# Performance work log

Hardware: AMD Instinct MI355X
Metric: run time of the kernel (lower is better)

Reference implementation:

```python
import jax, jax.numpy as jnp
import numpy as np

EMB = 128
EA = 32
ET = 32
NN = 50000
NE = 320000
NBAND = 3
LAM = 0.01  # softshrink sparsity_threshold
LN_EPS = 1e-5


def _softshrink(x, lam=LAM):
    return jnp.where(x > lam, x - lam, jnp.where(x < -lam, x + lam, jnp.zeros_like(x)))


def _forward(hidden, edge_attr, edge_time_emb, boundary_condition,
             alpha, r1, i1, rb1, ib1, fre_w, fre_b,
             comb_w, comb_b, lin_w, lin_b, ln_g, ln_b, edge_index):
    num_nodes = hidden.shape[0]
    # gather source node features and concat edge features -> [E, d_in]
    x = jnp.concatenate([hidden[edge_index[0]], edge_attr, edge_time_emb], axis=1)
    # FreMLP: FFT over feature dim (real input -> complex64)
    x_fft = jnp.fft.fft(x)
    xr, xi = x_fft.real, x_fft.imag
    energy = jnp.sum(xr * xr + xi * xi, axis=-1)  # [E]
    energy_sum = jnp.sum(energy)
    outs = []
    for k in range(NBAND):
        factor = (2.0 * (k + 1) - 1.0) / (2.0 * NBAND)
        Qk = alpha[k] * factor * energy_sum
        bk = energy_sum / (alpha[k] * (2.0 * NBAND))
        mask = ((energy >= Qk - bk) & (energy <= Qk + bk)).astype(x.dtype)[:, None]
        fr = xr * mask
        fi = xi * mask
        # complex linear: (fr + i*fi) @ (r1 + i*i1) + (rb1 + i*ib1)
        o_r = fr @ r1[k] - fi @ i1[k] + rb1[k]
        o_i = fi @ r1[k] + fr @ i1[k] + ib1[k]
        o_r = _softshrink(jax.nn.relu(o_r))
        o_i = _softshrink(jax.nn.relu(o_i))
        outs.append(jax.lax.complex(o_r, o_i))
    y_fft = jnp.concatenate(outs, axis=-1)  # [E, NBAND*EMB] complex
    y = jnp.fft.ifft(y_fft).real
    msg = y @ fre_w + fre_b  # [E, EMB]
    # view_as_complex(msg, 0) -> view_as_real -> flatten: interleave real with zeros
    msg_ri = jnp.stack([msg, jnp.zeros_like(msg)], axis=-1).reshape(msg.shape[0], 2 * EMB)
    msg2 = msg_ri @ comb_w + comb_b  # [E, EMB]
    # scatter-reduce(sum) into destination nodes + boundary self-loops
    msg_aug = jnp.concatenate([msg2, boundary_condition], axis=0)
    idx_aug = jnp.concatenate([edge_index[1], jnp.arange(num_nodes, dtype=edge_index.dtype)])
    out = jax.ops.segment_sum(msg_aug, idx_aug, num_segments=num_nodes)
    out = out @ lin_w + lin_b
    mu = jnp.mean(out, axis=-1, keepdims=True)
    var = jnp.mean((out - mu) ** 2, axis=-1, keepdims=True)
    out = (out - mu) * jax.lax.rsqrt(var + LN_EPS) * ln_g + ln_b
    return jax.nn.relu(out)  # dropout is identity in eval mode


def setup_inputs() -> dict:
    key = jax.random.key(0)
    ks = jax.random.split(key, 16)
    d_in = EMB + EA + ET
    s = 0.02
    return {
        "hidden": jax.random.normal(ks[0], (NN, EMB), jnp.float32),
        "edge_attr": jax.random.normal(ks[1], (NE, EA), jnp.float32),
        "edge_time_emb": jax.random.normal(ks[2], (NE, ET), jnp.float32),
        "boundary_condition": jax.random.normal(ks[3], (NN, EMB), jnp.float32),
        "alpha": jnp.ones((NBAND,), jnp.float32),
        "r1": s * jax.random.normal(ks[4], (NBAND, d_in, EMB), jnp.float32),
        "i1": s * jax.random.normal(ks[5], (NBAND, d_in, EMB), jnp.float32),
        "rb1": s * jax.random.normal(ks[6], (NBAND, EMB), jnp.float32),
        "ib1": s * jax.random.normal(ks[7], (NBAND, EMB), jnp.float32),
        "fre_w": s * jax.random.normal(ks[8], (NBAND * EMB, EMB), jnp.float32),
        "fre_b": s * jax.random.normal(ks[9], (EMB,), jnp.float32),
        "comb_w": s * jax.random.normal(ks[10], (2 * EMB, EMB), jnp.float32),
        "comb_b": s * jax.random.normal(ks[11], (EMB,), jnp.float32),
        "lin_w": s * jax.random.normal(ks[12], (EMB, EMB), jnp.float32),
        "lin_b": s * jax.random.normal(ks[13], (EMB,), jnp.float32),
        "ln_g": jnp.ones((EMB,), jnp.float32),
        "ln_b": jnp.zeros((EMB,), jnp.float32),
        "edge_index": jax.random.randint(ks[14], (2, NE), 0, NN, dtype=jnp.int32),
    }


def reference(hidden, edge_attr, edge_time_emb, boundary_condition, alpha, r1, i1, rb1, ib1,
              fre_w, fre_b, comb_w, comb_b, lin_w, lin_b, ln_g, ln_b, edge_index):
    return _forward(hidden, edge_attr, edge_time_emb, boundary_condition, alpha, r1, i1,
                    rb1, ib1, fre_w, fre_b, comb_w, comb_b, lin_w, lin_b, ln_g, ln_b, edge_index)
```

## Files before the change

kernel.cpp:

```cpp
#include <hip/hip_runtime.h>
#include <hip/hip_bf16.h>

#define NNODES 50000
#define NEDGES 320000
#define EMB 128
#define DIN 192
#define NB 3
#define LAM 0.01f
#define LN_EPS 1e-5f
#define PI_F 3.14159265358979323846f

#define SCAN_B 196
#define SCAN_N (SCAN_B * 256)

typedef __attribute__((ext_vector_type(8))) short v8s;
typedef __attribute__((ext_vector_type(4))) float v4f;
typedef __attribute__((ext_vector_type(2))) float v2f;

#define WS_ESUM 0
#define WS_WB   16
#define WS_G2B  (WS_WB + 73728)
#define WS_G2   (WS_G2B + 49152)
#define WS_PHI  (WS_G2 + 98304)
#define WS_M    (WS_PHI + 98304)
#define WS_BB   (WS_M + 16384)
#define WS_GB2  (WS_BB + 768)
#define WS_CK   (WS_GB2 + 128)
#define WS_EN   (WS_CK + 384)
#define WS_NORM (WS_EN + NEDGES)
#define WS_CNT  (WS_NORM + NNODES)
#define WS_CUR  (WS_CNT + SCAN_N)
#define WS_PART (WS_CUR + SCAN_N)
#define WS_EIDS (WS_PART + 256)

__device__ __forceinline__ unsigned pk2(float a, float b) {
  __hip_bfloat162 h2 = __float22bfloat162_rn(make_float2(a, b));
  return *reinterpret_cast<unsigned*>(&h2);
}

__device__ __forceinline__ void atomic2(float* dp, float a, float b) {
#if __has_builtin(__builtin_amdgcn_flat_atomic_fadd_v2f32)
  v2f val; val.x = a; val.y = b;
  __builtin_amdgcn_flat_atomic_fadd_v2f32((v2f*)dp, val);
#else
  atomicAdd(dp, a); atomicAdd(dp + 1, b);
#endif
}

__global__ __launch_bounds__(256) void k_prep1(
    const float* __restrict__ r1, const float* __restrict__ i1,
    __hip_bfloat16* __restrict__ Wb, const float* __restrict__ comb_w,
    const float* __restrict__ lin_w, float* __restrict__ M,
    const float* __restrict__ fre_w, float* __restrict__ Phi,
    const float* __restrict__ hidden, float* __restrict__ norms) {
  __shared__ float cs[384], sn[384];
  const int t = threadIdx.x;
  const int b = blockIdx.x;
  if (b < 576) {
    if (t < 192) sincosf((2.f * PI_F / 192.f) * (float)t, &sn[t], &cs[t]);
    __syncthreads();
    int idx = b * 256 + t;
    int n = idx / 768, c = idx - (idx / 768) * 768;
    int k = c >> 8, col = c & 255;
    int isI = col >> 7, j = col & 127;
    const float* ap = (isI ? i1 : r1) + (size_t)k * DIN * EMB + j;
    const float* bp = (isI ? r1 : i1) + (size_t)k * DIN * EMB + j;
    float sgn = isI ? -1.f : 1.f;
    float acc = 0.f;
    int m = 0;
    for (int f = 0; f < DIN; ++f) {
      acc = fmaf(cs[m], ap[(size_t)f * EMB], fmaf(sgn * sn[m], bp[(size_t)f * EMB], acc));
      m += n; if (m >= 192) m -= 192;
    }
    int kc = n >> 5, quad = (n & 31) >> 3, jj = n & 7;
    int lane = quad * 16 + (col & 15);
    Wb[((((k * 6 + kc) * 16 + (col >> 4)) * 64) + lane) * 8 + jj] = __float2bfloat16(acc);
  } else if (b < 640) {
    int idx = (b - 576) * 256 + t;
    int j = idx >> 7, j2 = idx & 127;
    float acc = 0.f;
    for (int tt = 0; tt < 128; ++tt)
      acc = fmaf(comb_w[(2 * j) * 128 + tt], lin_w[tt * 128 + j2], acc);
    M[idx] = acc;
  } else if (b < 1024) {
    for (int i = t; i < 384; i += 256)
      sincosf((2.f * PI_F / 384.f) * (float)i, &sn[i], &cs[i]);
    __syncthreads();
    int idx = (b - 640) * 256 + t;
    int slot = idx >> 7, j1 = idx & 127;
    int k = slot >> 8, r = slot & 255;
    int isI = r >> 7;
    int f = k * 128 + (r & 127);
    const float* tp = isI ? sn : cs;
    float sg = isI ? -1.f : 1.f;
    float acc = 0.f;
    int m = 0;
    for (int n = 0; n < 384; ++n) {
      acc = fmaf(sg * tp[m], fre_w[n * 128 + j1], acc);
      m += f; if (m >= 384) m -= 384;
    }
    Phi[slot * 128 + j1] = acc * (1.f / 384.f);
  } else {
    const int w = t >> 6, lane = t & 63;
    const int n = (b - 1024) * 4 + w;
    const float2 v = ((const float2*)(hidden + (size_t)n * 128))[lane];
    float ss = v.x * v.x + v.y * v.y;
#pragma unroll
    for (int off = 32; off > 0; off >>= 1) ss += __shfl_xor(ss, off, 64);
    if (lane == 0) norms[n] = ss;
  }
}

__global__ __launch_bounds__(256) void k_prep2(
    const float* __restrict__ Phi, const float* __restrict__ M,
    float* __restrict__ G2, __hip_bfloat16* __restrict__ G2b,
    const float* __restrict__ norms, const float* __restrict__ eattr,
    const float* __restrict__ ett, const int* __restrict__ eidx,
    float* __restrict__ energies, float* __restrict__ esum,
    int* __restrict__ cnt) {
  const int t = threadIdx.x;
  const int b = blockIdx.x;
  if (b < 384) {
    int idx = b * 256 + t;
    int slot = idx >> 7, j2 = idx & 127;
    float acc = 0.f;
    for (int j1 = 0; j1 < 128; ++j1)
      acc = fmaf(Phi[slot * 128 + j1], M[j1 * 128 + j2], acc);
    G2[idx] = acc;
    int k = slot >> 8, s = slot & 255;
    int kc = s >> 5, quad = (s & 31) >> 3, jj = s & 7;
    G2b[((((k * 8 + kc) * 8 + (j2 >> 4)) * 64) + quad * 16 + (j2 & 15)) * 8 + jj] =
        __float2bfloat16(acc);
  } else {
    int e = (b - 384) * 256 + t;
    float ss = norms[eidx[e]];
    const float4* a4 = (const float4*)(eattr + (size_t)e * 32);
#pragma unroll
    for (int i = 0; i < 8; ++i) {
      float4 v = a4[i];
      ss += v.x * v.x + v.y * v.y + v.z * v.z + v.w * v.w;
    }
    const float4* t4 = (const float4*)(ett + (size_t)e * 32);
#pragma unroll
    for (int i = 0; i < 8; ++i) {
      float4 v = t4[i];
      ss += v.x * v.x + v.y * v.y + v.z * v.z + v.w * v.w;
    }
    float en = 192.f * ss;
    energies[e] = en;
    float tot = en;
#pragma unroll
    for (int off = 32; off > 0; off >>= 1) tot += __shfl_down(tot, off, 64);
    if ((t & 63) == 0) atomicAdd(esum, tot);
    atomicAdd(&cnt[eidx[NEDGES + e]], 1);
  }
}

__global__ __launch_bounds__(256) void k_prep3(
    const float* __restrict__ rb1, const float* __restrict__ ib1,
    const float* __restrict__ fre_b, const float* __restrict__ comb_b,
    const float* __restrict__ lin_w, const float* __restrict__ M,
    const float* __restrict__ G2, float* __restrict__ bb,
    float* __restrict__ gb2, float* __restrict__ ck,
    int* __restrict__ cnt, int* __restrict__ part) {
  __shared__ int sm[256];
  const int t = threadIdx.x;
  const int b = blockIdx.x;
  if (b < 5) {
    int idx = b * 256 + t;
    if (idx < 768) {
      int k = idx >> 8, r = idx & 255;
      bb[idx] = (r >= 128) ? ib1[k * 128 + (r & 127)] : rb1[k * 128 + r];
    } else if (idx < 896) {
      int j2 = idx - 768;
      float acc = 0.f;
      for (int j = 0; j < 128; ++j) acc += fre_b[j] * M[j * 128 + j2];
      for (int tt = 0; tt < 128; ++tt) acc += comb_b[tt] * lin_w[tt * 128 + j2];
      gb2[j2] = acc;
    } else if (idx < 1280) {
      int q = idx - 896;
      int k = q >> 7, j2 = q & 127;
      float acc = 0.f;
      for (int j = 0; j < 128; ++j) {
        float vr = rb1[k * 128 + j];
        vr = fmaxf(vr, 0.f); vr = (vr > LAM) ? vr - LAM : 0.f;
        float vi = ib1[k * 128 + j];
        vi = fmaxf(vi, 0.f); vi = (vi > LAM) ? vi - LAM : 0.f;
        acc += vr * G2[(k * 256 + j) * 128 + j2] + vi * G2[(k * 256 + 128 + j) * 128 + j2];
      }
      ck[k * 128 + j2] = acc;
    }
  } else {
    int blk = b - 5;
    int i = blk * 256 + t;
    int v = (i < NNODES) ? cnt[i] : 0;
    sm[t] = v;
    __syncthreads();
#pragma unroll
    for (int off = 1; off < 256; off <<= 1) {
      int x = (t >= off) ? sm[t - off] : 0;
      __syncthreads();
      sm[t] += x;
      __syncthreads();
    }
    cnt[i] = sm[t] - v;
    if (t == 255) part[blk] = sm[t];
  }
}

__global__ __launch_bounds__(256) void k_scanB(int* __restrict__ part) {
  __shared__ int sm[256];
  const int t = threadIdx.x;
  int v = (t < SCAN_B) ? part[t] : 0;
  sm[t] = v;
  __syncthreads();
#pragma unroll
  for (int off = 1; off < 256; off <<= 1) {
    int x = (t >= off) ? sm[t - off] : 0;
    __syncthreads();
    sm[t] += x;
    __syncthreads();
  }
  if (t < SCAN_B) part[t] = sm[t] - v;
}

__global__ __launch_bounds__(256) void k_scanC(const int* __restrict__ scanned,
                                               const int* __restrict__ part,
                                               int* __restrict__ cur) {
  int i = blockIdx.x * 256 + threadIdx.x;
  cur[i] = scanned[i] + part[blockIdx.x];
}

__global__ __launch_bounds__(256) void k_fill(const int* __restrict__ eidx,
                                              int* __restrict__ cur,
                                              int* __restrict__ eids) {
  int e = blockIdx.x * 256 + threadIdx.x;
  int pos = atomicAdd(&cur[eidx[NEDGES + e]], 1);
  eids[pos] = e;
}

#define XS_STR 200
#define OS_STR 264
#define ZS_STR 130
__global__ __launch_bounds__(512, 4) void k_edges(
    const float* __restrict__ hidden, const float* __restrict__ eattr,
    const float* __restrict__ ett, const float* __restrict__ alpha,
    const int* __restrict__ eidx, const int* __restrict__ eids,
    const __hip_bfloat16* __restrict__ Wb, const __hip_bfloat16* __restrict__ G2b,
    const float* __restrict__ bb, const float* __restrict__ gb2,
    const float* __restrict__ ck, const float* __restrict__ energies,
    const float* __restrict__ esum, float* __restrict__ accum) {
  __shared__ __align__(16) char smem[64 * XS_STR * 2 + 64 * OS_STR * 2];
  short* Xs = (short*)smem;
  short* Os = (short*)(smem + 64 * XS_STR * 2);
  float* Zs = (float*)smem;
  __shared__ float maskf[3][64];
  __shared__ int eid_s[64], srcs[64], dsts[64];
  __shared__ int tileact[3];

  const int t = threadIdx.x;
  const int e0 = blockIdx.x * 64;
  const int lane = t & 63, w = t >> 6;
  const int quad = lane >> 4, lc = lane & 15;

  if (t < 3) tileact[t] = 0;
  if (t < 64) {
    int eid = eids[e0 + t];
    eid_s[t] = eid;
    srcs[t] = eidx[eid];
    dsts[t] = eidx[NEDGES + eid];
    float en = energies[eid];
    float es = *esum;
#pragma unroll
    for (int k = 0; k < NB; ++k) {
      float a = alpha[k];
      float factor = (2.f * (k + 1) - 1.f) / (2.f * NB);
      float Q = a * factor * es;
      float b = es / (a * (2.f * NB));
      bool m = (en >= Q - b) && (en <= Q + b);
      maskf[k][t] = m ? 1.f : 0.f;
      if (m) atomicOr(&tileact[k], 1);
    }
  }
  __syncthreads();

#pragma unroll
  for (int it = 0; it < 4; ++it) {
    int i = t + it * 512;
    int e = i >> 5, c4 = i & 31;
    const float4 v = *(const float4*)(hidden + (size_t)srcs[e] * 128 + c4 * 4);
    unsigned* p = (unsigned*)&Xs[e * XS_STR + c4 * 4];
    p[0] = pk2(v.x, v.y); p[1] = pk2(v.z, v.w);
  }
#pragma unroll
  for (int it = 0; it < 2; ++it) {
    int i = t + it * 512;
    int e = i >> 4, q = i & 15;
    float4 v;
    if (q < 8) v = ((const float4*)(eattr + (size_t)eid_s[e] * 32))[q];
    else       v = ((const float4*)(ett + (size_t)eid_s[e] * 32))[q - 8];
    unsigned* p = (unsigned*)&Xs[e * XS_STR + 128 + q * 4];
    p[0] = pk2(v.x, v.y); p[1] = pk2(v.z, v.w);
  }
  __syncthreads();

  v4f acc2[4];
#pragma unroll
  for (int mt = 0; mt < 4; ++mt)
#pragma unroll
    for (int r = 0; r < 4; ++r) acc2[mt][r] = 0.f;

  for (int k = 0; k < NB; ++k) {
    if (!tileact[k]) continue;
    v4f accA[4][2];
#pragma unroll
    for (int mt = 0; mt < 4; ++mt)
#pragma unroll
      for (int n = 0; n < 2; ++n)
#pragma unroll
        for (int r = 0; r < 4; ++r) accA[mt][n][r] = 0.f;

#pragma unroll
    for (int kc = 0; kc < 6; ++kc) {
      v8s af[4];
#pragma unroll
      for (int mt = 0; mt < 4; ++mt)
        af[mt] = *(const v8s*)&Xs[(mt * 16 + lc) * XS_STR + kc * 32 + quad * 8];
      const __hip_bfloat16* wp = Wb + ((((k * 6 + kc) * 16 + 2 * w) * 64) + lane) * 8;
#pragma unroll
      for (int ntl = 0; ntl < 2; ++ntl) {
        v8s bfr = *(const v8s*)(const void*)(wp + ntl * 512);
#pragma unroll
        for (int mt = 0; mt < 4; ++mt)
          accA[mt][ntl] =
              __builtin_amdgcn_mfma_f32_16x16x32_bf16(af[mt], bfr, accA[mt][ntl], 0, 0, 0);
      }
    }
    __syncthreads();
#pragma unroll
    for (int mt = 0; mt < 4; ++mt)
#pragma unroll
      for (int ntl = 0; ntl < 2; ++ntl) {
        int col = w * 32 + ntl * 16 + lc;
        float bbv = bb[k * 256 + col];
#pragma unroll
        for (int reg = 0; reg < 4; ++reg) {
          int row = mt * 16 + quad * 4 + reg;
          float mk = maskf[k][row];
          float v = fmaf(mk, accA[mt][ntl][reg], bbv);
          v = fmaxf(v, 0.f);
          v = (v > LAM) ? v - LAM : 0.f;
          __hip_bfloat16 h = __float2bfloat16(v);
          Os[row * OS_STR + col] = *reinterpret_cast<short*>(&h);
        }
      }
    __syncthreads();
#pragma unroll
    for (int kc = 0; kc < 8; ++kc) {
      v8s of[4];
#pragma unroll
      for (int mt = 0; mt < 4; ++mt)
        of[mt] = *(const v8s*)&Os[(mt * 16 + lc) * OS_STR + kc * 32 + quad * 8];
      const __hip_bfloat16* gp = G2b + ((((k * 8 + kc) * 8 + w) * 64) + lane) * 8;
      v8s bfr = *(const v8s*)(const void*)gp;
#pragma unroll
      for (int mt = 0; mt < 4; ++mt)
        acc2[mt] = __builtin_amdgcn_mfma_f32_16x16x32_bf16(of[mt], bfr, acc2[mt], 0, 0, 0);
    }
  }

  __syncthreads();
  {
    int col = w * 16 + lc;
    float base = gb2[col];
#pragma unroll
    for (int k = 0; k < NB; ++k)
      if (!tileact[k]) base += ck[k * 128 + col];
#pragma unroll
    for (int mt = 0; mt < 4; ++mt)
#pragma unroll
      for (int reg = 0; reg < 4; ++reg) {
        int row = mt * 16 + quad * 4 + reg;
        Zs[row * ZS_STR + col] = acc2[mt][reg] + base;
      }
  }
  __syncthreads();
  if (w < 2) {
    int c = 2 * lane;
    int r0 = w * 32;
    float s0 = 0.f, s1 = 0.f;
#pragma unroll
    for (int r = 0; r < 32; ++r) {
      int row = r0 + r;
      s0 += Zs[row * ZS_STR + c];
      s1 += Zs[row * ZS_STR + c + 1];
      int d = dsts[row];
      if (r == 31 || dsts[row + 1] != d) {
        atomic2(accum + (size_t)d * 128 + c, s0, s1);
        s0 = 0.f; s1 = 0.f;
      }
    }
  }
}

__global__ __launch_bounds__(256) void k_nodes(const float* __restrict__ boundary,
                                               const float* __restrict__ lin_w,
                                               const float* __restrict__ lin_b,
                                               const float* __restrict__ ln_g,
                                               const float* __restrict__ ln_b,
                                               float* __restrict__ out) {
  __shared__ float lw[32][128];
  const int t = threadIdx.x;
  const int w = t >> 6, lane = t & 63;
  const int n = blockIdx.x * 4 + w;
  float a0 = out[(size_t)n * 128 + lane] + lin_b[lane];
  float a1 = out[(size_t)n * 128 + 64 + lane] + lin_b[64 + lane];
  for (int cb = 0; cb < 128; cb += 32) {
    __syncthreads();
#pragma unroll
    for (int it = 0; it < 16; ++it) {
      int i = t + it * 256;
      lw[i >> 7][i & 127] = lin_w[(cb + (i >> 7)) * 128 + (i & 127)];
    }
    __syncthreads();
#pragma unroll
    for (int r = 0; r < 32; ++r) {
      float bv = boundary[(size_t)n * 128 + cb + r];
      a0 = fmaf(bv, lw[r][lane], a0);
      a1 = fmaf(bv, lw[r][64 + lane], a1);
    }
  }
  float s = a0 + a1, sq = a0 * a0 + a1 * a1;
#pragma unroll
  for (int off = 32; off > 0; off >>= 1) {
    s += __shfl_xor(s, off, 64);
    sq += __shfl_xor(sq, off, 64);
  }
  float mu = s * (1.f / 128.f);
  float var = sq * (1.f / 128.f) - mu * mu;
  float rs = 1.f / sqrtf(var + LN_EPS);
  float y0 = (a0 - mu) * rs * ln_g[lane] + ln_b[lane];
  float y1 = (a1 - mu) * rs * ln_g[64 + lane] + ln_b[64 + lane];
  out[(size_t)n * 128 + lane] = fmaxf(y0, 0.f);
  out[(size_t)n * 128 + 64 + lane] = fmaxf(y1, 0.f);
}

extern "C" void kernel_launch(void* const* d_in, const int* in_sizes, int n_in,
                              void* d_out, int out_size, void* d_ws, size_t ws_size,
                              hipStream_t stream) {
  const float* hidden   = (const float*)d_in[0];
  const float* eattr    = (const float*)d_in[1];
  const float* ett      = (const float*)d_in[2];
  const float* boundary = (const float*)d_in[3];
  const float* alpha    = (const float*)d_in[4];
  const float* r1       = (const float*)d_in[5];
  const float* i1       = (const float*)d_in[6];
  const float* rb1      = (const float*)d_in[7];
  const float* ib1      = (const float*)d_in[8];
  const float* fre_w    = (const float*)d_in[9];
  const float* fre_b    = (const float*)d_in[10];
  const float* comb_w   = (const float*)d_in[11];
  const float* comb_b   = (const float*)d_in[12];
  const float* lin_w    = (const float*)d_in[13];
  const float* lin_b    = (const float*)d_in[14];
  const float* ln_g     = (const float*)d_in[15];
  const float* ln_b     = (const float*)d_in[16];
  const int*   eidx     = (const int*)d_in[17];
  float* ws  = (float*)d_ws;
  float* out = (float*)d_out;
  __hip_bfloat16* Wb  = (__hip_bfloat16*)(ws + WS_WB);
  __hip_bfloat16* G2b = (__hip_bfloat16*)(ws + WS_G2B);
  int* cnt  = (int*)(ws + WS_CNT);
  int* cur  = (int*)(ws + WS_CUR);
  int* part = (int*)(ws + WS_PART);
  int* eids = (int*)(ws + WS_EIDS);

  hipMemsetAsync(ws + WS_ESUM, 0, 16 * sizeof(float), stream);
  hipMemsetAsync(cnt, 0, SCAN_N * sizeof(int), stream);
  hipMemsetAsync(out, 0, (size_t)NNODES * EMB * sizeof(float), stream);

  k_prep1<<<1024 + 12500, 256, 0, stream>>>(r1, i1, Wb, comb_w, lin_w, ws + WS_M,
                                            fre_w, ws + WS_PHI, hidden, ws + WS_NORM);
  k_prep2<<<384 + NEDGES / 256, 256, 0, stream>>>(ws + WS_PHI, ws + WS_M, ws + WS_G2,
                                                  G2b, ws + WS_NORM, eattr, ett, eidx,
                                                  ws + WS_EN, ws + WS_ESUM, cnt);
  k_prep3<<<5 + SCAN_B, 256, 0, stream>>>(rb1, ib1, fre_b, comb_b, lin_w, ws + WS_M,
                                          ws + WS_G2, ws + WS_BB, ws + WS_GB2,
                                          ws + WS_CK, cnt, part);
  k_scanB<<<1, 256, 0, stream>>>(part);
  k_scanC<<<SCAN_B, 256, 0, stream>>>(cnt, part, cur);
  k_fill<<<NEDGES / 256, 256, 0, stream>>>(eidx, cur, eids);
  k_edges<<<NEDGES / 64, 512, 0, stream>>>(hidden, eattr, ett, alpha, eidx, eids,
                                           Wb, G2b, ws + WS_BB, ws + WS_GB2,
                                           ws + WS_CK, ws + WS_EN, ws + WS_ESUM, out);
  k_nodes<<<NNODES / 4, 256, 0, stream>>>(boundary, lin_w, lin_b, ln_g, ln_b, out);
}
```

Before: 553.3 us.

## Fold memsets and prep kernels, use decoupled-lookback scan, prefetch edge loads

```diff
diff --git a/kernel.cpp b/kernel.cpp
--- a/kernel.cpp
+++ b/kernel.cpp
@@ -20,8 +20,7 @@
 #define WS_ESUM 0
 #define WS_WB   16
 #define WS_G2B  (WS_WB + 73728)
-#define WS_G2   (WS_G2B + 49152)
-#define WS_PHI  (WS_G2 + 98304)
+#define WS_PHI  (WS_G2B + 49152)
 #define WS_M    (WS_PHI + 98304)
 #define WS_BB   (WS_M + 16384)
 #define WS_GB2  (WS_BB + 768)
@@ -30,8 +29,8 @@
 #define WS_NORM (WS_EN + NEDGES)
 #define WS_CNT  (WS_NORM + NNODES)
 #define WS_CUR  (WS_CNT + SCAN_N)
-#define WS_PART (WS_CUR + SCAN_N)
-#define WS_EIDS (WS_PART + 256)
+#define WS_LOOK (WS_CUR + SCAN_N)
+#define WS_EIDS (WS_LOOK + 512)
 
 __device__ __forceinline__ unsigned pk2(float a, float b) {
   __hip_bfloat162 h2 = __float22bfloat162_rn(make_float2(a, b));
@@ -47,16 +46,23 @@
 #endif
 }
 
+#define P1_WF   576
+#define P1_M    (P1_WF + 64)
+#define P1_PHI  (P1_M + 384)
+#define P1_NORM (P1_PHI + 12500)
+#define P1_ZOUT (P1_NORM + 6250)
+#define P1_ZCNT (P1_ZOUT + SCAN_B)
 __global__ __launch_bounds__(256) void k_prep1(
     const float* __restrict__ r1, const float* __restrict__ i1,
     __hip_bfloat16* __restrict__ Wb, const float* __restrict__ comb_w,
     const float* __restrict__ lin_w, float* __restrict__ M,
     const float* __restrict__ fre_w, float* __restrict__ Phi,
-    const float* __restrict__ hidden, float* __restrict__ norms) {
+    const float* __restrict__ hidden, float* __restrict__ norms,
+    float* __restrict__ out, int* __restrict__ cnt, float* __restrict__ esum) {
   __shared__ float cs[384], sn[384];
   const int t = threadIdx.x;
   const int b = blockIdx.x;
-  if (b < 576) {
+  if (b < P1_WF) {
     if (t < 192) sincosf((2.f * PI_F / 192.f) * (float)t, &sn[t], &cs[t]);
     __syncthreads();
     int idx = b * 256 + t;
@@ -75,18 +81,18 @@
     int kc = n >> 5, quad = (n & 31) >> 3, jj = n & 7;
     int lane = quad * 16 + (col & 15);
     Wb[((((k * 6 + kc) * 16 + (col >> 4)) * 64) + lane) * 8 + jj] = __float2bfloat16(acc);
-  } else if (b < 640) {
-    int idx = (b - 576) * 256 + t;
+  } else if (b < P1_M) {
+    int idx = (b - P1_WF) * 256 + t;
     int j = idx >> 7, j2 = idx & 127;
     float acc = 0.f;
     for (int tt = 0; tt < 128; ++tt)
       acc = fmaf(comb_w[(2 * j) * 128 + tt], lin_w[tt * 128 + j2], acc);
     M[idx] = acc;
-  } else if (b < 1024) {
+  } else if (b < P1_PHI) {
     for (int i = t; i < 384; i += 256)
       sincosf((2.f * PI_F / 384.f) * (float)i, &sn[i], &cs[i]);
     __syncthreads();
-    int idx = (b - 640) * 256 + t;
+    int idx = (b - P1_M) * 256 + t;
     int slot = idx >> 7, j1 = idx & 127;
     int k = slot >> 8, r = slot & 255;
     int isI = r >> 7;
@@ -100,39 +106,52 @@
       m += f; if (m >= 384) m -= 384;
     }
     Phi[slot * 128 + j1] = acc * (1.f / 384.f);
-  } else {
+  } else if (b < P1_NORM) {
     const int w = t >> 6, lane = t & 63;
-    const int n = (b - 1024) * 4 + w;
+    const int n = (b - P1_PHI) * 4 + w;
     const float2 v = ((const float2*)(hidden + (size_t)n * 128))[lane];
     float ss = v.x * v.x + v.y * v.y;
 #pragma unroll
     for (int off = 32; off > 0; off >>= 1) ss += __shfl_xor(ss, off, 64);
     if (lane == 0) norms[n] = ss;
-  }
-}
-
+  } else if (b < P1_ZOUT) {
+    int idx = (b - P1_NORM) * 256 + t;
+    ((float4*)out)[idx] = make_float4(0.f, 0.f, 0.f, 0.f);
+  } else {
+    int idx = (b - P1_ZOUT) * 256 + t;
+    cnt[idx] = 0;
+    if (b == P1_ZOUT && t < 16) esum[t] = 0.f;
+  }
+}
+
+#define P2_G2  384
+#define P2_EN  (P2_G2 + 1250)
+#define P2_BB  (P2_EN + 5)
 __global__ __launch_bounds__(256) void k_prep2(
     const float* __restrict__ Phi, const float* __restrict__ M,
-    float* __restrict__ G2, __hip_bfloat16* __restrict__ G2b,
-    const float* __restrict__ norms, const float* __restrict__ eattr,
-    const float* __restrict__ ett, const int* __restrict__ eidx,
-    float* __restrict__ energies, float* __restrict__ esum,
-    int* __restrict__ cnt) {
+    __hip_bfloat16* __restrict__ G2b, const float* __restrict__ norms,
+    const float* __restrict__ eattr, const float* __restrict__ ett,
+    const int* __restrict__ eidx, float* __restrict__ energies,
+    float* __restrict__ esum, int* __restrict__ cnt,
+    const float* __restrict__ rb1, const float* __restrict__ ib1,
+    const float* __restrict__ fre_b, const float* __restrict__ comb_b,
+    const float* __restrict__ lin_w, float* __restrict__ bb,
+    float* __restrict__ gb2, float* __restrict__ ck,
+    unsigned long long* __restrict__ look) {
   const int t = threadIdx.x;
   const int b = blockIdx.x;
-  if (b < 384) {
+  if (b < P2_G2) {
     int idx = b * 256 + t;
     int slot = idx >> 7, j2 = idx & 127;
     float acc = 0.f;
     for (int j1 = 0; j1 < 128; ++j1)
       acc = fmaf(Phi[slot * 128 + j1], M[j1 * 128 + j2], acc);
-    G2[idx] = acc;
     int k = slot >> 8, s = slot & 255;
     int kc = s >> 5, quad = (s & 31) >> 3, jj = s & 7;
     G2b[((((k * 8 + kc) * 8 + (j2 >> 4)) * 64) + quad * 16 + (j2 & 15)) * 8 + jj] =
         __float2bfloat16(acc);
-  } else {
-    int e = (b - 384) * 256 + t;
+  } else if (b < P2_EN) {
+    int e = (b - P2_G2) * 256 + t;
     float ss = norms[eidx[e]];
     const float4* a4 = (const float4*)(eattr + (size_t)e * 32);
 #pragma unroll
@@ -153,21 +172,8 @@
     for (int off = 32; off > 0; off >>= 1) tot += __shfl_down(tot, off, 64);
     if ((t & 63) == 0) atomicAdd(esum, tot);
     atomicAdd(&cnt[eidx[NEDGES + e]], 1);
-  }
-}
-
-__global__ __launch_bounds__(256) void k_prep3(
-    const float* __restrict__ rb1, const float* __restrict__ ib1,
-    const float* __restrict__ fre_b, const float* __restrict__ comb_b,
-    const float* __restrict__ lin_w, const float* __restrict__ M,
-    const float* __restrict__ G2, float* __restrict__ bb,
-    float* __restrict__ gb2, float* __restrict__ ck,
-    int* __restrict__ cnt, int* __restrict__ part) {
-  __shared__ int sm[256];
-  const int t = threadIdx.x;
-  const int b = blockIdx.x;
-  if (b < 5) {
-    int idx = b * 256 + t;
+  } else if (b < P2_BB) {
+    int idx = (b - P2_EN) * 256 + t;
     if (idx < 768) {
       int k = idx >> 8, r = idx & 255;
       bb[idx] = (r >= 128) ? ib1[k * 128 + (r & 127)] : rb1[k * 128 + r];
@@ -177,41 +183,48 @@
       for (int j = 0; j < 128; ++j) acc += fre_b[j] * M[j * 128 + j2];
       for (int tt = 0; tt < 128; ++tt) acc += comb_b[tt] * lin_w[tt * 128 + j2];
       gb2[j2] = acc;
-    } else if (idx < 1280) {
-      int q = idx - 896;
-      int k = q >> 7, j2 = q & 127;
-      float acc = 0.f;
-      for (int j = 0; j < 128; ++j) {
-        float vr = rb1[k * 128 + j];
-        vr = fmaxf(vr, 0.f); vr = (vr > LAM) ? vr - LAM : 0.f;
-        float vi = ib1[k * 128 + j];
-        vi = fmaxf(vi, 0.f); vi = (vi > LAM) ? vi - LAM : 0.f;
-        acc += vr * G2[(k * 256 + j) * 128 + j2] + vi * G2[(k * 256 + 128 + j) * 128 + j2];
-      }
-      ck[k * 128 + j2] = acc;
+    } else if (idx < 1152) {
+      look[idx - 896] = 0ULL;
     }
   } else {
-    int blk = b - 5;
-    int i = blk * 256 + t;
-    int v = (i < NNODES) ? cnt[i] : 0;
-    sm[t] = v;
-    __syncthreads();
-#pragma unroll
-    for (int off = 1; off < 256; off <<= 1) {
-      int x = (t >= off) ? sm[t - off] : 0;
-      __syncthreads();
-      sm[t] += x;
-      __syncthreads();
-    }
-    cnt[i] = sm[t] - v;
-    if (t == 255) part[blk] = sm[t];
-  }
-}
-
-__global__ __launch_bounds__(256) void k_scanB(int* __restrict__ part) {
+    __shared__ float ckphi[NB][128];
+    if (t < 128) {
+#pragma unroll
+      for (int k = 0; k < NB; ++k) {
+        float acc = 0.f;
+        for (int j = 0; j < 128; ++j) {
+          float vr = rb1[k * 128 + j];
+          vr = fmaxf(vr, 0.f); vr = (vr > LAM) ? vr - LAM : 0.f;
+          float vi = ib1[k * 128 + j];
+          vi = fmaxf(vi, 0.f); vi = (vi > LAM) ? vi - LAM : 0.f;
+          acc += vr * Phi[(k * 256 + j) * 128 + t] +
+                 vi * Phi[(k * 256 + 128 + j) * 128 + t];
+        }
+        ckphi[k][t] = acc;
+      }
+    }
+    __syncthreads();
+    if (t < 128) {
+#pragma unroll
+      for (int k = 0; k < NB; ++k) {
+        float acc = 0.f;
+        for (int j1 = 0; j1 < 128; ++j1)
+          acc = fmaf(ckphi[k][j1], M[j1 * 128 + t], acc);
+        ck[k * 128 + t] = acc;
+      }
+    }
+  }
+}
+
+__global__ __launch_bounds__(256) void k_scan(const int* __restrict__ cnt,
+                                              int* __restrict__ cur,
+                                              unsigned long long* __restrict__ look) {
   __shared__ int sm[256];
+  __shared__ int xoff;
   const int t = threadIdx.x;
-  int v = (t < SCAN_B) ? part[t] : 0;
+  const int b = blockIdx.x;
+  int i = b * 256 + t;
+  int v = cnt[i];
   sm[t] = v;
   __syncthreads();
 #pragma unroll
@@ -221,14 +234,33 @@
     sm[t] += x;
     __syncthreads();
   }
-  if (t < SCAN_B) part[t] = sm[t] - v;
-}
-
-__global__ __launch_bounds__(256) void k_scanC(const int* __restrict__ scanned,
-                                               const int* __restrict__ part,
-                                               int* __restrict__ cur) {
-  int i = blockIdx.x * 256 + threadIdx.x;
-  cur[i] = scanned[i] + part[blockIdx.x];
+  if (t == 0) {
+    int total = sm[255];
+    if (b == 0) {
+      __hip_atomic_store(&look[0], (2ULL << 32) | (unsigned)total,
+                         __ATOMIC_RELEASE, __HIP_MEMORY_SCOPE_AGENT);
+      xoff = 0;
+    } else {
+      __hip_atomic_store(&look[b], (1ULL << 32) | (unsigned)total,
+                         __ATOMIC_RELEASE, __HIP_MEMORY_SCOPE_AGENT);
+      unsigned run = 0;
+      int p = b - 1;
+      while (true) {
+        unsigned long long s = __hip_atomic_load(&look[p], __ATOMIC_ACQUIRE,
+                                                 __HIP_MEMORY_SCOPE_AGENT);
+        unsigned st = (unsigned)(s >> 32);
+        if (st == 0) { __builtin_amdgcn_s_sleep(8); continue; }
+        run += (unsigned)s;
+        if (st == 2) break;
+        --p;
+      }
+      __hip_atomic_store(&look[b], (2ULL << 32) | (unsigned)(run + (unsigned)total),
+                         __ATOMIC_RELEASE, __HIP_MEMORY_SCOPE_AGENT);
+      xoff = (int)run;
+    }
+  }
+  __syncthreads();
+  cur[i] = sm[t] - v + xoff;
 }
 
 __global__ __launch_bounds__(256) void k_fill(const int* __restrict__ eidx,
@@ -263,6 +295,14 @@
   const int lane = t & 63, w = t >> 6;
   const int quad = lane >> 4, lc = lane & 15;
 
+  v8s wpre[12];
+#pragma unroll
+  for (int kc = 0; kc < 6; ++kc)
+#pragma unroll
+    for (int ntl = 0; ntl < 2; ++ntl)
+      wpre[kc * 2 + ntl] =
+          *(const v8s*)(const void*)(Wb + (((kc * 16 + 2 * w + ntl) * 64) + lane) * 8);
+
   if (t < 3) tileact[t] = 0;
   if (t < 64) {
     int eid = eids[e0 + t];
@@ -284,23 +324,32 @@
   }
   __syncthreads();
 
-#pragma unroll
-  for (int it = 0; it < 4; ++it) {
-    int i = t + it * 512;
-    int e = i >> 5, c4 = i & 31;
-    const float4 v = *(const float4*)(hidden + (size_t)srcs[e] * 128 + c4 * 4);
-    unsigned* p = (unsigned*)&Xs[e * XS_STR + c4 * 4];
-    p[0] = pk2(v.x, v.y); p[1] = pk2(v.z, v.w);
-  }
-#pragma unroll
-  for (int it = 0; it < 2; ++it) {
-    int i = t + it * 512;
-    int e = i >> 4, q = i & 15;
-    float4 v;
-    if (q < 8) v = ((const float4*)(eattr + (size_t)eid_s[e] * 32))[q];
-    else       v = ((const float4*)(ett + (size_t)eid_s[e] * 32))[q - 8];
-    unsigned* p = (unsigned*)&Xs[e * XS_STR + 128 + q * 4];
-    p[0] = pk2(v.x, v.y); p[1] = pk2(v.z, v.w);
+  {
+    float4 hv[4]; int he[4], hc[4];
+#pragma unroll
+    for (int it = 0; it < 4; ++it) {
+      int i = t + it * 512;
+      he[it] = i >> 5; hc[it] = i & 31;
+      hv[it] = *(const float4*)(hidden + (size_t)srcs[he[it]] * 128 + hc[it] * 4);
+    }
+    float4 fv[2]; int fe[2], fq[2];
+#pragma unroll
+    for (int it = 0; it < 2; ++it) {
+      int i = t + it * 512;
+      fe[it] = i >> 4; fq[it] = i & 15;
+      if (fq[it] < 8) fv[it] = ((const float4*)(eattr + (size_t)eid_s[fe[it]] * 32))[fq[it]];
+      else            fv[it] = ((const float4*)(ett + (size_t)eid_s[fe[it]] * 32))[fq[it] - 8];
+    }
+#pragma unroll
+    for (int it = 0; it < 4; ++it) {
+      unsigned* p = (unsigned*)&Xs[he[it] * XS_STR + hc[it] * 4];
+      p[0] = pk2(hv[it].x, hv[it].y); p[1] = pk2(hv[it].z, hv[it].w);
+    }
+#pragma unroll
+    for (int it = 0; it < 2; ++it) {
+      unsigned* p = (unsigned*)&Xs[fe[it] * XS_STR + 128 + fq[it] * 4];
+      p[0] = pk2(fv[it].x, fv[it].y); p[1] = pk2(fv[it].z, fv[it].w);
+    }
   }
   __syncthreads();
 
@@ -310,6 +359,7 @@
 #pragma unroll
     for (int r = 0; r < 4; ++r) acc2[mt][r] = 0.f;
 
+#pragma unroll
   for (int k = 0; k < NB; ++k) {
     if (!tileact[k]) continue;
     v4f accA[4][2];
@@ -329,7 +379,8 @@
       const __hip_bfloat16* wp = Wb + ((((k * 6 + kc) * 16 + 2 * w) * 64) + lane) * 8;
 #pragma unroll
       for (int ntl = 0; ntl < 2; ++ntl) {
-        v8s bfr = *(const v8s*)(const void*)(wp + ntl * 512);
+        v8s bfr = (k == 0) ? wpre[kc * 2 + ntl]
+                           : *(const v8s*)(const void*)(wp + ntl * 512);
 #pragma unroll
         for (int mt = 0; mt < 4; ++mt)
           accA[mt][ntl] =
@@ -472,23 +523,17 @@
   __hip_bfloat16* G2b = (__hip_bfloat16*)(ws + WS_G2B);
   int* cnt  = (int*)(ws + WS_CNT);
   int* cur  = (int*)(ws + WS_CUR);
-  int* part = (int*)(ws + WS_PART);
+  unsigned long long* look = (unsigned long long*)(ws + WS_LOOK);
   int* eids = (int*)(ws + WS_EIDS);
 
-  hipMemsetAsync(ws + WS_ESUM, 0, 16 * sizeof(float), stream);
-  hipMemsetAsync(cnt, 0, SCAN_N * sizeof(int), stream);
-  hipMemsetAsync(out, 0, (size_t)NNODES * EMB * sizeof(float), stream);
-
-  k_prep1<<<1024 + 12500, 256, 0, stream>>>(r1, i1, Wb, comb_w, lin_w, ws + WS_M,
-                                            fre_w, ws + WS_PHI, hidden, ws + WS_NORM);
-  k_prep2<<<384 + NEDGES / 256, 256, 0, stream>>>(ws + WS_PHI, ws + WS_M, ws + WS_G2,
-                                                  G2b, ws + WS_NORM, eattr, ett, eidx,
-                                                  ws + WS_EN, ws + WS_ESUM, cnt);
-  k_prep3<<<5 + SCAN_B, 256, 0, stream>>>(rb1, ib1, fre_b, comb_b, lin_w, ws + WS_M,
-                                          ws + WS_G2, ws + WS_BB, ws + WS_GB2,
-                                          ws + WS_CK, cnt, part);
-  k_scanB<<<1, 256, 0, stream>>>(part);
-  k_scanC<<<SCAN_B, 256, 0, stream>>>(cnt, part, cur);
+  k_prep1<<<P1_ZCNT, 256, 0, stream>>>(r1, i1, Wb, comb_w, lin_w, ws + WS_M,
+                                       fre_w, ws + WS_PHI, hidden, ws + WS_NORM,
+                                       out, cnt, ws + WS_ESUM);
+  k_prep2<<<P2_BB + 1, 256, 0, stream>>>(ws + WS_PHI, ws + WS_M, G2b, ws + WS_NORM,
+                                         eattr, ett, eidx, ws + WS_EN, ws + WS_ESUM,
+                                         cnt, rb1, ib1, fre_b, comb_b, lin_w,
+                                         ws + WS_BB, ws + WS_GB2, ws + WS_CK, look);
+  k_scan<<<SCAN_B, 256, 0, stream>>>(cnt, cur, look);
   k_fill<<<NEDGES / 256, 256, 0, stream>>>(eidx, cur, eids);
   k_edges<<<NEDGES / 64, 512, 0, stream>>>(hidden, eattr, ett, alpha, eidx, eids,
                                            Wb, G2b, ws + WS_BB, ws + WS_GB2,
```

Measured after the change: 559.0 us. About the same (+1.0%).
